# Kernel optimization log

Hardware: AMD Instinct MI355X
Metric: run time of the kernel (lower is better)

## Reference

```python
import jax, jax.numpy as jnp
import numpy as np


def gcn_conv(x, src, dst, W, b, num_nodes):
    # PyG GCNConv: add self-loops, symmetric deg^-1/2 normalization, scatter-add.
    h = x @ W                                    # [N, out]
    loops = jnp.arange(num_nodes, dtype=src.dtype)
    s = jnp.concatenate([src, loops])            # [E+N]
    d = jnp.concatenate([dst, loops])            # [E+N]
    deg = jax.ops.segment_sum(jnp.ones_like(d, dtype=h.dtype), d, num_segments=num_nodes)
    dinv = jnp.where(deg > 0, jax.lax.rsqrt(deg), 0.0)
    norm = dinv[s] * dinv[d]                     # [E+N]
    msgs = h[s] * norm[:, None]                  # gather + scale  [E+N, out]
    out = jax.ops.segment_sum(msgs, d, num_segments=num_nodes)
    return out + b


NUM_GRAPHS = 512


def setup_inputs() -> dict:
    key = jax.random.key(0)
    ks = jax.random.split(key, 12)
    N, E, F = 50000, 400000, 128
    x = jax.random.normal(ks[0], (N, F), dtype=jnp.float32)
    edge_index = jax.random.randint(ks[1], (2, E), 0, N, dtype=jnp.int64)
    batch = jnp.sort(jax.random.randint(ks[2], (N,), 0, NUM_GRAPHS, dtype=jnp.int64))
    def lin(k, fi, fo):
        return jax.random.normal(k, (fi, fo), dtype=jnp.float32) * (1.0 / np.sqrt(fi))
    return {
        "x": x, "edge_index": edge_index, "batch": batch,
        "W1": lin(ks[3], F, 512), "b1": jnp.zeros((512,), jnp.float32),
        "W2": lin(ks[4], 512, 256), "b2": jnp.zeros((256,), jnp.float32),
        "W3": lin(ks[5], 256, 128), "b3": jnp.zeros((128,), jnp.float32),
        "W4": lin(ks[6], 128, 32), "b4": jnp.zeros((32,), jnp.float32),
        "W5": lin(ks[7], 32, 10), "b5": jnp.zeros((10,), jnp.float32),
    }


def reference(x, edge_index, batch, W1, b1, W2, b2, W3, b3, W4, b4, W5, b5):
    N = x.shape[0]
    src, dst = edge_index[0], edge_index[1]
    h = gcn_conv(x, src, dst, W1, b1, N)
    h = jax.nn.leaky_relu(h, negative_slope=0.01)
    h = gcn_conv(h, src, dst, W2, b2, N)          # [N, 256]
    embs = jax.ops.segment_max(h, batch, num_segments=NUM_GRAPHS)  # [G, 256]
    z = ((h @ W3 + b3) @ W4 + b4) @ W5 + b5       # [N, 10]
    out = jax.ops.segment_max(z, batch, num_segments=NUM_GRAPHS)   # [G, 10]
    return (out, embs)
```

## Files before the change

kernel.cpp:

```cpp
#include <hip/hip_runtime.h>
#include <math.h>

#define DIV_UP(a,b) (((a)+(b)-1)/(b))

typedef __attribute__((ext_vector_type(8))) short bf16x8;
typedef __attribute__((ext_vector_type(4))) float f32x4;

__device__ inline unsigned short f2b(float x) {
    unsigned int u = __float_as_uint(x);
    u += 0x7fffu + ((u >> 16) & 1u);
    return (unsigned short)(u >> 16);
}

__device__ inline void cvt8(uint4 v, float* a) {
    a[0] = __uint_as_float(v.x << 16); a[1] = __uint_as_float(v.x & 0xffff0000u);
    a[2] = __uint_as_float(v.y << 16); a[3] = __uint_as_float(v.y & 0xffff0000u);
    a[4] = __uint_as_float(v.z << 16); a[5] = __uint_as_float(v.z & 0xffff0000u);
    a[6] = __uint_as_float(v.w << 16); a[7] = __uint_as_float(v.w & 0xffff0000u);
}

__device__ inline void gl16(void* lds, const void* g) {
    __builtin_amdgcn_global_load_lds(
        (const __attribute__((address_space(1))) void*)g,
        (__attribute__((address_space(3))) void*)lds, 16, 0, 0);
}

__global__ void k_zero_i(int* p, int n) {
    int i = blockIdx.x * blockDim.x + threadIdx.x;
    if (i < n) p[i] = 0;
}

__global__ void k_hist(const int* __restrict__ dst, int* __restrict__ hist, int E) {
    int i = blockIdx.x * blockDim.x + threadIdx.x;
    if (i < E) atomicAdd(&hist[dst[i]], 1);
}

__global__ __launch_bounds__(256) void k_scan_bsum(const int* __restrict__ hist,
                                                   int* __restrict__ bsum, int N) {
    __shared__ int red[256];
    int t = threadIdx.x;
    int base = blockIdx.x * 1024 + t * 4;
    int s = 0;
    if (base + 3 < N) {
        int4 v = *(const int4*)&hist[base];
        s = v.x + v.y + v.z + v.w;
    } else {
        for (int j = 0; j < 4; ++j) if (base + j < N) s += hist[base + j];
    }
    red[t] = s;
    __syncthreads();
    for (int off = 128; off >= 1; off >>= 1) {
        if (t < off) red[t] += red[t + off];
        __syncthreads();
    }
    if (t == 0) bsum[blockIdx.x] = red[0];
}

__global__ __launch_bounds__(1024) void k_scan_boff(const int* __restrict__ bsum,
        int* __restrict__ boff, int* __restrict__ row_off, int NB, int N) {
    __shared__ int s[1024];
    int t = threadIdx.x;
    int v = (t < NB) ? bsum[t] : 0;
    s[t] = v;
    __syncthreads();
    for (int off = 1; off < 1024; off <<= 1) {
        int u = (t >= off) ? s[t - off] : 0;
        __syncthreads();
        s[t] += u;
        __syncthreads();
    }
    if (t < NB) boff[t] = s[t] - v;
    if (t == NB - 1) row_off[N] = s[t];
}

__global__ __launch_bounds__(256) void k_scan_apply(const int* __restrict__ hist,
        const int* __restrict__ boff, int* __restrict__ row_off,
        float* __restrict__ dinv, int N) {
    __shared__ int s[256];
    int t = threadIdx.x;
    int base = blockIdx.x * 1024 + t * 4;
    int v[4];
    int loc = 0;
#pragma unroll
    for (int j = 0; j < 4; ++j) { v[j] = (base + j < N) ? hist[base + j] : 0; loc += v[j]; }
    s[t] = loc;
    __syncthreads();
    for (int off = 1; off < 256; off <<= 1) {
        int u = (t >= off) ? s[t - off] : 0;
        __syncthreads();
        s[t] += u;
        __syncthreads();
    }
    int run = boff[blockIdx.x] + s[t] - loc;
#pragma unroll
    for (int j = 0; j < 4; ++j) {
        if (base + j < N) {
            row_off[base + j] = run;
            dinv[base + j] = rsqrtf((float)(v[j] + 1));
        }
        run += v[j];
    }
}

__global__ void k_bin(const int* __restrict__ src, const int* __restrict__ dst,
                      const int* __restrict__ row_off, int* __restrict__ cursor,
                      const float* __restrict__ dinv,
                      int* __restrict__ csr_src, float* __restrict__ csr_w, int E) {
    int i = blockIdx.x * blockDim.x + threadIdx.x;
    if (i >= E) return;
    int d = dst[i], s = src[i];
    int pos = row_off[d] + atomicAdd(&cursor[d], 1);
    csr_src[pos] = s;
    csr_w[pos] = dinv[s] * dinv[d];
}

__global__ void k_bounds(const int* __restrict__ batch, int* __restrict__ bounds,
                         int N, int G) {
    int g = blockIdx.x * blockDim.x + threadIdx.x;
    if (g > G) return;
    int lo = 0, hi = N;
    while (lo < hi) { int mid = (lo + hi) >> 1; if (batch[mid] < g) lo = mid + 1; else hi = mid; }
    bounds[g] = lo;
}

__global__ void k_prep(const float* __restrict__ x, unsigned short* __restrict__ xb, int n4,
                       const float* __restrict__ W1, unsigned short* __restrict__ w1t,
                       int K1, int N1,
                       const float* __restrict__ W2, unsigned short* __restrict__ w2t,
                       int K2, int N2) {
    int i = blockIdx.x * blockDim.x + threadIdx.x;
    if (i < n4) {
        float4 v = ((const float4*)x)[i];
        ushort4 o;
        o.x = f2b(v.x); o.y = f2b(v.y); o.z = f2b(v.z); o.w = f2b(v.w);
        ((ushort4*)xb)[i] = o;
        return;
    }
    i -= n4;
    if (i < K1 * N1) {
        int k = i / N1, n = i % N1;
        w1t[(size_t)n * K1 + k] = f2b(W1[i]);
        return;
    }
    i -= K1 * N1;
    if (i < K2 * N2) {
        int k = i / N2, n = i % N2;
        w2t[(size_t)n * K2 + k] = f2b(W2[i]);
    }
}

__global__ __launch_bounds__(256) void k_wc(const float* __restrict__ W3,
        const float* __restrict__ W4, const float* __restrict__ W5,
        const float* __restrict__ b3, const float* __restrict__ b4,
        const float* __restrict__ b5, float* __restrict__ WcT, float* __restrict__ bc) {
    int c = blockIdx.x;
    int t = threadIdx.x;
    if (c < 10) {
        __shared__ float Tc[128];
        if (t < 128) {
            float s = 0.f;
#pragma unroll 8
            for (int k = 0; k < 32; ++k) s = fmaf(W4[t * 32 + k], W5[k * 10 + c], s);
            Tc[t] = s;
        }
        __syncthreads();
        float s = 0.f;
        const float* w3r = &W3[t * 128];
#pragma unroll 8
        for (int j = 0; j < 128; ++j) s = fmaf(w3r[j], Tc[j], s);
        WcT[c * 256 + t] = s;
    } else {
        __shared__ float v[32];
        if (t < 32) {
            float s = b4[t];
            for (int j = 0; j < 128; ++j) s = fmaf(b3[j], W4[j * 32 + t], s);
            v[t] = s;
        }
        __syncthreads();
        if (t < 10) {
            float s = b5[t];
            for (int k = 0; k < 32; ++k) s = fmaf(v[k], W5[k * 10 + t], s);
            bc[t] = s;
        }
    }
}

template <int F>
__global__ __launch_bounds__(256) void k_gather_b(const unsigned short* __restrict__ H,
        const int* __restrict__ row_off, const int* __restrict__ csr_src,
        const float* __restrict__ csr_w, const float* __restrict__ dinv,
        const float* __restrict__ bias, unsigned short* __restrict__ outb, int N) {
    const int LPN = F / 8;
    const int NPB = 256 / LPN;
    int node = blockIdx.x * NPB + threadIdx.x / LPN;
    if (node >= N) return;
    int f = (threadIdx.x % LPN) * 8;
    const unsigned short* Hf = H + f;
    float sc = dinv[node]; sc *= sc;
    float a[8];
    cvt8(*(const uint4*)&Hf[(size_t)node * F], a);
#pragma unroll
    for (int j = 0; j < 8; ++j) a[j] *= sc;
    if (bias) {
#pragma unroll
        for (int j = 0; j < 8; ++j) a[j] += bias[f + j];
    }
    int e0 = row_off[node], e1 = row_off[node + 1];
    int e = e0;
    for (; e + 4 <= e1; e += 4) {
        int s0 = csr_src[e + 0], s1 = csr_src[e + 1];
        int s2 = csr_src[e + 2], s3 = csr_src[e + 3];
        uint4 v0 = *(const uint4*)&Hf[(size_t)s0 * F];
        uint4 v1 = *(const uint4*)&Hf[(size_t)s1 * F];
        uint4 v2 = *(const uint4*)&Hf[(size_t)s2 * F];
        uint4 v3 = *(const uint4*)&Hf[(size_t)s3 * F];
        float w0 = csr_w[e + 0], w1 = csr_w[e + 1];
        float w2 = csr_w[e + 2], w3 = csr_w[e + 3];
        float b0[8], b1[8], b2[8], b3[8];
        cvt8(v0, b0); cvt8(v1, b1); cvt8(v2, b2); cvt8(v3, b3);
#pragma unroll
        for (int j = 0; j < 8; ++j) {
            a[j] = fmaf(w0, b0[j], a[j]);
            a[j] = fmaf(w1, b1[j], a[j]);
            a[j] = fmaf(w2, b2[j], a[j]);
            a[j] = fmaf(w3, b3[j], a[j]);
        }
    }
    for (; e < e1; ++e) {
        int s = csr_src[e];
        float w = csr_w[e];
        float b[8];
        cvt8(*(const uint4*)&Hf[(size_t)s * F], b);
#pragma unroll
        for (int j = 0; j < 8; ++j) a[j] = fmaf(w, b[j], a[j]);
    }
    uint4 o;
    o.x = (unsigned)f2b(a[0]) | ((unsigned)f2b(a[1]) << 16);
    o.y = (unsigned)f2b(a[2]) | ((unsigned)f2b(a[3]) << 16);
    o.z = (unsigned)f2b(a[4]) | ((unsigned)f2b(a[5]) << 16);
    o.w = (unsigned)f2b(a[6]) | ((unsigned)f2b(a[7]) << 16);
    *(uint4*)&outb[(size_t)node * F + f] = o;
}

template <int OUT_BF16, int ACT>
__global__ __launch_bounds__(256) void k_gemm_mfma(const unsigned short* __restrict__ A,
        const unsigned short* __restrict__ Bt, const float* __restrict__ bias,
        void* __restrict__ Cout, int M, int K, int NC) {
    __shared__ __align__(16) unsigned short As[128][64];
    __shared__ __align__(16) unsigned short Bs[128][64];
    int tid = threadIdx.x;
    int wave = tid >> 6, lane = tid & 63;
    int row0 = blockIdx.y * 128, col0 = blockIdx.x * 128;
    int wr = (wave >> 1) * 64, wc = (wave & 1) * 64;
    f32x4 acc[4][4] = {};
    int lr = lane & 15;
    int lg = lane >> 4;
    int sw = ((lane & 7) ^ (lane >> 3)) << 3;
    int ch0 = (lg ^ (lr & 7)) << 3;
    int ch1 = ch0 ^ (4 << 3);

    for (int k0 = 0; k0 < K; k0 += 64) {
#pragma unroll
        for (int c = 0; c < 4; ++c) {
            int rl = wave * 32 + c * 8 + (lane >> 3);
            int gr = min(row0 + rl, M - 1);
            gl16(&As[wave * 32 + c * 8][0], &A[(size_t)gr * K + k0 + sw]);
            gl16(&Bs[wave * 32 + c * 8][0], &Bt[(size_t)(col0 + rl) * K + k0 + sw]);
        }
        __syncthreads();
        bf16x8 af[2][4], bv[2][4];
#pragma unroll
        for (int i = 0; i < 4; ++i) {
            int ra = wr + i * 16 + lr;
            int rb = wc + i * 16 + lr;
            af[0][i] = *(const bf16x8*)&As[ra][ch0];
            af[1][i] = *(const bf16x8*)&As[ra][ch1];
            bv[0][i] = *(const bf16x8*)&Bs[rb][ch0];
            bv[1][i] = *(const bf16x8*)&Bs[rb][ch1];
        }
#pragma unroll
        for (int s = 0; s < 2; ++s)
#pragma unroll
            for (int i = 0; i < 4; ++i)
#pragma unroll
                for (int j = 0; j < 4; ++j)
                    acc[i][j] = __builtin_amdgcn_mfma_f32_16x16x32_bf16(bv[s][j], af[s][i], acc[i][j], 0, 0, 0);
        __syncthreads();
    }

    int q4 = lg * 4;
    float4 bb[4];
#pragma unroll
    for (int j = 0; j < 4; ++j)
        bb[j] = bias ? *(const float4*)&bias[col0 + wc + j * 16 + q4]
                     : make_float4(0.f, 0.f, 0.f, 0.f);
#pragma unroll
    for (int i = 0; i < 4; ++i) {
        int row = row0 + wr + i * 16 + lr;
        if (row >= M) continue;
#pragma unroll
        for (int j = 0; j < 4; ++j) {
            int c0 = col0 + wc + j * 16 + q4;
            float4 v;
            v.x = acc[i][j][0] + bb[j].x;
            v.y = acc[i][j][1] + bb[j].y;
            v.z = acc[i][j][2] + bb[j].z;
            v.w = acc[i][j][3] + bb[j].w;
            if (ACT) {
                v.x = (v.x >= 0.f) ? v.x : 0.01f * v.x;
                v.y = (v.y >= 0.f) ? v.y : 0.01f * v.y;
                v.z = (v.z >= 0.f) ? v.z : 0.01f * v.z;
                v.w = (v.w >= 0.f) ? v.w : 0.01f * v.w;
            }
            if (OUT_BF16) {
                uint2 o;
                o.x = (unsigned)f2b(v.x) | ((unsigned)f2b(v.y) << 16);
                o.y = (unsigned)f2b(v.z) | ((unsigned)f2b(v.w) << 16);
                *(uint2*)&((unsigned short*)Cout)[(size_t)row * NC + c0] = o;
            } else {
                *(float4*)&((float*)Cout)[(size_t)row * NC + c0] = v;
            }
        }
    }
}

__global__ __launch_bounds__(320) void k_head_segmax(const unsigned short* __restrict__ H,
        const float* __restrict__ WcT, const float* __restrict__ bc,
        const int* __restrict__ bounds, float* __restrict__ out,
        float* __restrict__ out_emb) {
    __shared__ __align__(16) float Ws[10][260];
    __shared__ float bs[10];
    __shared__ float red[320];
    int t = threadIdx.x;
    for (int i = t; i < 2560; i += 320) Ws[i / 256][i % 256] = WcT[i];
    if (t < 10) bs[t] = bc[t];
    __syncthreads();
    int g = blockIdx.x;
    int s = bounds[g], e = bounds[g + 1];
    int col = t % 10, rs = t / 10;
    float m = -INFINITY;
    for (int r = s + rs; r < e; r += 32) {
        const unsigned short* hr = &H[(size_t)r * 256];
        float acc = bs[col];
#pragma unroll 4
        for (int k = 0; k < 256; k += 8) {
            float h[8];
            cvt8(*(const uint4*)&hr[k], h);
            float4 wa = *(const float4*)&Ws[col][k];
            float4 wb = *(const float4*)&Ws[col][k + 4];
            acc = fmaf(h[0], wa.x, acc);
            acc = fmaf(h[1], wa.y, acc);
            acc = fmaf(h[2], wa.z, acc);
            acc = fmaf(h[3], wa.w, acc);
            acc = fmaf(h[4], wb.x, acc);
            acc = fmaf(h[5], wb.y, acc);
            acc = fmaf(h[6], wb.z, acc);
            acc = fmaf(h[7], wb.w, acc);
        }
        m = fmaxf(m, acc);
    }
    red[t] = m;
    __syncthreads();
    for (int step = 16; step >= 1; step >>= 1) {
        if (rs < step) red[rs * 10 + col] = fmaxf(red[rs * 10 + col], red[(rs + step) * 10 + col]);
        __syncthreads();
    }
    if (rs == 0) out[(size_t)g * 10 + col] = red[col];
    if (t < 256) {
        float mm = -INFINITY;
        for (int r = s; r < e; ++r)
            mm = fmaxf(mm, __uint_as_float(((unsigned)H[(size_t)r * 256 + t]) << 16));
        out_emb[(size_t)g * 256 + t] = mm;
    }
}

extern "C" void kernel_launch(void* const* d_in, const int* in_sizes, int n_in,
                              void* d_out, int out_size, void* d_ws, size_t ws_size,
                              hipStream_t stream) {
    const float* x  = (const float*)d_in[0];
    const int* ei   = (const int*)d_in[1];
    const int* batch= (const int*)d_in[2];
    const float* W1 = (const float*)d_in[3];
    const float* b1 = (const float*)d_in[4];
    const float* W2 = (const float*)d_in[5];
    const float* b2 = (const float*)d_in[6];
    const float* W3 = (const float*)d_in[7];
    const float* b3 = (const float*)d_in[8];
    const float* W4 = (const float*)d_in[9];
    const float* b4 = (const float*)d_in[10];
    const float* W5 = (const float*)d_in[11];
    const float* b5 = (const float*)d_in[12];

    const int N  = in_sizes[2];
    const int F  = in_sizes[0] / N;
    const int E  = in_sizes[1] / 2;
    const int C1 = in_sizes[4];
    const int C2 = in_sizes[6];
    const int C5 = in_sizes[12];
    const int G  = out_size / (C2 + C5);
    const int NB = DIV_UP(N, 1024);

    const int* srcp = ei;
    const int* dstp = ei + E;

    uintptr_t p = (uintptr_t)d_ws;
    auto carve = [&](size_t bytes) {
        uintptr_t r = p;
        p += (bytes + 255) & ~(size_t)255;
        return (void*)r;
    };
    int* hist    = (int*)carve(sizeof(int) * N);
    int* cursor  = (int*)carve(sizeof(int) * N);
    int* row_off = (int*)carve(sizeof(int) * (N + 1));
    int* bounds  = (int*)carve(sizeof(int) * (G + 1));
    int* bsum    = (int*)carve(sizeof(int) * NB);
    int* boff    = (int*)carve(sizeof(int) * NB);
    int* csr_src = (int*)carve(sizeof(int) * E);
    float* csr_w = (float*)carve(sizeof(float) * E);
    float* dinv  = (float*)carve(sizeof(float) * N);
    float* wct   = (float*)carve(sizeof(float) * C2 * C5);
    float* bcv   = (float*)carve(sizeof(float) * C5);
    unsigned short* w1t = (unsigned short*)carve(sizeof(short) * F * C1);
    unsigned short* w2t = (unsigned short*)carve(sizeof(short) * C1 * C2);
    unsigned short* xb    = (unsigned short*)carve(sizeof(short) * (size_t)N * F);
    unsigned short* aggxb = (unsigned short*)carve(sizeof(short) * (size_t)N * F);
    unsigned short* h1b   = (unsigned short*)carve(sizeof(short) * (size_t)N * C1);
    unsigned short* t2b   = (unsigned short*)carve(sizeof(short) * (size_t)N * C2);
    unsigned short* h2b   = (unsigned short*)carve(sizeof(short) * (size_t)N * C2);

    float* out     = (float*)d_out;
    float* out_emb = out + (size_t)G * C5;

    int zspan = (int)(((sizeof(int) * N + 255) & ~(size_t)255) / 4) + N;
    k_zero_i<<<DIV_UP(zspan, 256), 256, 0, stream>>>(hist, zspan);
    k_hist<<<DIV_UP(E, 256), 256, 0, stream>>>(dstp, hist, E);
    k_scan_bsum<<<NB, 256, 0, stream>>>(hist, bsum, N);
    k_scan_boff<<<1, 1024, 0, stream>>>(bsum, boff, row_off, NB, N);
    k_scan_apply<<<NB, 256, 0, stream>>>(hist, boff, row_off, dinv, N);
    k_bin<<<DIV_UP(E, 256), 256, 0, stream>>>(srcp, dstp, row_off, cursor, dinv,
                                              csr_src, csr_w, E);
    k_bounds<<<DIV_UP(G + 1, 256), 256, 0, stream>>>(batch, bounds, N, G);
    k_wc<<<11, 256, 0, stream>>>(W3, W4, W5, b3, b4, b5, wct, bcv);

    int n4 = N * F / 4;
    int prep_total = n4 + F * C1 + C1 * C2;
    k_prep<<<DIV_UP(prep_total, 256), 256, 0, stream>>>(x, xb, n4,
                                                        W1, w1t, F, C1,
                                                        W2, w2t, C1, C2);

    k_gather_b<128><<<DIV_UP(N, 16), 256, 0, stream>>>(
        xb, row_off, csr_src, csr_w, dinv, nullptr, aggxb, N);
    dim3 g1(C1 / 128, DIV_UP(N, 128));
    k_gemm_mfma<1, 1><<<g1, 256, 0, stream>>>(aggxb, w1t, b1, h1b, N, F, C1);

    dim3 g2(C2 / 128, DIV_UP(N, 128));
    k_gemm_mfma<1, 0><<<g2, 256, 0, stream>>>(h1b, w2t, nullptr, t2b, N, C1, C2);
    k_gather_b<256><<<DIV_UP(N, 8), 256, 0, stream>>>(
        t2b, row_off, csr_src, csr_w, dinv, b2, h2b, N);

    k_head_segmax<<<G, 320, 0, stream>>>(h2b, wct, bcv, bounds, out, out_emb);
}
```

Measured before the change: 310.4 us.

## Widen GEMM tile to 128x256 with 8 waves and merge small prep kernels

The MFMA GEMM now uses 512-thread blocks computing 128x256 output tiles, so each loaded A tile is reused across twice as many columns and fewer blocks are launched. Separately, the bounds, combined-weight and bf16 prep kernels are folded into a single launch to cut launch overhead. Larger blocks increase LDS use and may lower occupancy, and for C2=256 the grid has only one column of blocks.

```diff
diff --git a/kernel.cpp b/kernel.cpp
--- a/kernel.cpp
+++ b/kernel.cpp
@@ -114,21 +114,58 @@
     csr_w[pos] = dinv[s] * dinv[d];
 }
 
-__global__ void k_bounds(const int* __restrict__ batch, int* __restrict__ bounds,
-                         int N, int G) {
-    int g = blockIdx.x * blockDim.x + threadIdx.x;
-    if (g > G) return;
-    int lo = 0, hi = N;
-    while (lo < hi) { int mid = (lo + hi) >> 1; if (batch[mid] < g) lo = mid + 1; else hi = mid; }
-    bounds[g] = lo;
-}
-
-__global__ void k_prep(const float* __restrict__ x, unsigned short* __restrict__ xb, int n4,
-                       const float* __restrict__ W1, unsigned short* __restrict__ w1t,
-                       int K1, int N1,
-                       const float* __restrict__ W2, unsigned short* __restrict__ w2t,
-                       int K2, int N2) {
-    int i = blockIdx.x * blockDim.x + threadIdx.x;
+__global__ __launch_bounds__(256) void k_pre(
+        const float* __restrict__ W3, const float* __restrict__ W4,
+        const float* __restrict__ W5, const float* __restrict__ b3,
+        const float* __restrict__ b4, const float* __restrict__ b5,
+        float* __restrict__ WcT, float* __restrict__ bc,
+        const int* __restrict__ batch, int* __restrict__ bounds, int N, int G, int nb,
+        const float* __restrict__ x, unsigned short* __restrict__ xb, int n4,
+        const float* __restrict__ W1, unsigned short* __restrict__ w1t, int K1, int N1,
+        const float* __restrict__ W2, unsigned short* __restrict__ w2t, int K2, int N2) {
+    int b = blockIdx.x;
+    int t = threadIdx.x;
+    if (b < 11) {
+        int c = b;
+        if (c < 10) {
+            __shared__ float Tc[128];
+            if (t < 128) {
+                float s = 0.f;
+#pragma unroll 8
+                for (int k = 0; k < 32; ++k) s = fmaf(W4[t * 32 + k], W5[k * 10 + c], s);
+                Tc[t] = s;
+            }
+            __syncthreads();
+            float s = 0.f;
+            const float* w3r = &W3[t * 128];
+#pragma unroll 8
+            for (int j = 0; j < 128; ++j) s = fmaf(w3r[j], Tc[j], s);
+            WcT[c * 256 + t] = s;
+        } else {
+            __shared__ float v[32];
+            if (t < 32) {
+                float s = b4[t];
+                for (int j = 0; j < 128; ++j) s = fmaf(b3[j], W4[j * 32 + t], s);
+                v[t] = s;
+            }
+            __syncthreads();
+            if (t < 10) {
+                float s = b5[t];
+                for (int k = 0; k < 32; ++k) s = fmaf(v[k], W5[k * 10 + t], s);
+                bc[t] = s;
+            }
+        }
+        return;
+    }
+    if (b < 11 + nb) {
+        int g = (b - 11) * 256 + t;
+        if (g > G) return;
+        int lo = 0, hi = N;
+        while (lo < hi) { int mid = (lo + hi) >> 1; if (batch[mid] < g) lo = mid + 1; else hi = mid; }
+        bounds[g] = lo;
+        return;
+    }
+    int i = (b - 11 - nb) * 256 + t;
     if (i < n4) {
         float4 v = ((const float4*)x)[i];
         ushort4 o;
@@ -146,42 +183,6 @@
     if (i < K2 * N2) {
         int k = i / N2, n = i % N2;
         w2t[(size_t)n * K2 + k] = f2b(W2[i]);
-    }
-}
-
-__global__ __launch_bounds__(256) void k_wc(const float* __restrict__ W3,
-        const float* __restrict__ W4, const float* __restrict__ W5,
-        const float* __restrict__ b3, const float* __restrict__ b4,
-        const float* __restrict__ b5, float* __restrict__ WcT, float* __restrict__ bc) {
-    int c = blockIdx.x;
-    int t = threadIdx.x;
-    if (c < 10) {
-        __shared__ float Tc[128];
-        if (t < 128) {
-            float s = 0.f;
-#pragma unroll 8
-            for (int k = 0; k < 32; ++k) s = fmaf(W4[t * 32 + k], W5[k * 10 + c], s);
-            Tc[t] = s;
-        }
-        __syncthreads();
-        float s = 0.f;
-        const float* w3r = &W3[t * 128];
-#pragma unroll 8
-        for (int j = 0; j < 128; ++j) s = fmaf(w3r[j], Tc[j], s);
-        WcT[c * 256 + t] = s;
-    } else {
-        __shared__ float v[32];
-        if (t < 32) {
-            float s = b4[t];
-            for (int j = 0; j < 128; ++j) s = fmaf(b3[j], W4[j * 32 + t], s);
-            v[t] = s;
-        }
-        __syncthreads();
-        if (t < 10) {
-            float s = b5[t];
-            for (int k = 0; k < 32; ++k) s = fmaf(v[k], W5[k * 10 + t], s);
-            bc[t] = s;
-        }
     }
 }
 
@@ -243,15 +244,15 @@
 }
 
 template <int OUT_BF16, int ACT>
-__global__ __launch_bounds__(256) void k_gemm_mfma(const unsigned short* __restrict__ A,
+__global__ __launch_bounds__(512) void k_gemm_mfma256(const unsigned short* __restrict__ A,
         const unsigned short* __restrict__ Bt, const float* __restrict__ bias,
         void* __restrict__ Cout, int M, int K, int NC) {
     __shared__ __align__(16) unsigned short As[128][64];
-    __shared__ __align__(16) unsigned short Bs[128][64];
+    __shared__ __align__(16) unsigned short Bs[256][64];
     int tid = threadIdx.x;
     int wave = tid >> 6, lane = tid & 63;
-    int row0 = blockIdx.y * 128, col0 = blockIdx.x * 128;
-    int wr = (wave >> 1) * 64, wc = (wave & 1) * 64;
+    int row0 = blockIdx.y * 128, col0 = blockIdx.x * 256;
+    int wr = (wave >> 2) * 64, wc = (wave & 3) * 64;
     f32x4 acc[4][4] = {};
     int lr = lane & 15;
     int lg = lane >> 4;
@@ -261,11 +262,15 @@
 
     for (int k0 = 0; k0 < K; k0 += 64) {
 #pragma unroll
+        for (int c = 0; c < 2; ++c) {
+            int rl = c * 64 + wave * 8 + (lane >> 3);
+            int gr = min(row0 + rl, M - 1);
+            gl16(&As[c * 64 + wave * 8][0], &A[(size_t)gr * K + k0 + sw]);
+        }
+#pragma unroll
         for (int c = 0; c < 4; ++c) {
-            int rl = wave * 32 + c * 8 + (lane >> 3);
-            int gr = min(row0 + rl, M - 1);
-            gl16(&As[wave * 32 + c * 8][0], &A[(size_t)gr * K + k0 + sw]);
-            gl16(&Bs[wave * 32 + c * 8][0], &Bt[(size_t)(col0 + rl) * K + k0 + sw]);
+            int rl = c * 64 + wave * 8 + (lane >> 3);
+            gl16(&Bs[c * 64 + wave * 8][0], &Bt[(size_t)(col0 + rl) * K + k0 + sw]);
         }
         __syncthreads();
         bf16x8 af[2][4], bv[2][4];
@@ -439,22 +444,22 @@
     k_scan_apply<<<NB, 256, 0, stream>>>(hist, boff, row_off, dinv, N);
     k_bin<<<DIV_UP(E, 256), 256, 0, stream>>>(srcp, dstp, row_off, cursor, dinv,
                                               csr_src, csr_w, E);
-    k_bounds<<<DIV_UP(G + 1, 256), 256, 0, stream>>>(batch, bounds, N, G);
-    k_wc<<<11, 256, 0, stream>>>(W3, W4, W5, b3, b4, b5, wct, bcv);
 
     int n4 = N * F / 4;
+    int nb_bounds = DIV_UP(G + 1, 256);
     int prep_total = n4 + F * C1 + C1 * C2;
-    k_prep<<<DIV_UP(prep_total, 256), 256, 0, stream>>>(x, xb, n4,
-                                                        W1, w1t, F, C1,
-                                                        W2, w2t, C1, C2);
+    int pre_blocks = 11 + nb_bounds + DIV_UP(prep_total, 256);
+    k_pre<<<pre_blocks, 256, 0, stream>>>(W3, W4, W5, b3, b4, b5, wct, bcv,
+                                          batch, bounds, N, G, nb_bounds,
+                                          x, xb, n4, W1, w1t, F, C1, W2, w2t, C1, C2);
 
     k_gather_b<128><<<DIV_UP(N, 16), 256, 0, stream>>>(
         xb, row_off, csr_src, csr_w, dinv, nullptr, aggxb, N);
-    dim3 g1(C1 / 128, DIV_UP(N, 128));
-    k_gemm_mfma<1, 1><<<g1, 256, 0, stream>>>(aggxb, w1t, b1, h1b, N, F, C1);
-
-    dim3 g2(C2 / 128, DIV_UP(N, 128));
-    k_gemm_mfma<1, 0><<<g2, 256, 0, stream>>>(h1b, w2t, nullptr, t2b, N, C1, C2);
+    dim3 g1(C1 / 256, DIV_UP(N, 128));
+    k_gemm_mfma256<1, 1><<<g1, 512, 0, stream>>>(aggxb, w1t, b1, h1b, N, F, C1);
+
+    dim3 g2(C2 / 256, DIV_UP(N, 128));
+    k_gemm_mfma256<1, 0><<<g2, 512, 0, stream>>>(h1b, w2t, nullptr, t2b, N, C1, C2);
     k_gather_b<256><<<DIV_UP(N, 8), 256, 0, stream>>>(
         t2b, row_off, csr_src, csr_w, dinv, b2, h2b, N);
 
```

New measurement: 286.4 us. -7.7%, faster.
